# Optimization experiments

Hardware: AMD Instinct MI355X
Metric: run time of the kernel (lower is better)

The kernel has to match this reference:

```python
import jax, jax.numpy as jnp
import numpy as np

B, DIM, H, W = 4, 512, 64, 64
HEADS = 8
MAX_FREQ = 10000.0


def _rope_cos_sin(h, w, head_dim, dtype):
    # 2D RoPE: first quarter of half_dim uses row position, second quarter uses col position
    half = head_dim // 2
    quarter = half // 2
    pos_h = jnp.arange(h, dtype=dtype)
    pos_w = jnp.arange(w, dtype=dtype)
    gh, gw = jnp.meshgrid(pos_h, pos_w, indexing='ij')
    pos = jnp.stack([gh.ravel(), gw.ravel()], axis=-1)  # [N, 2]
    freqs = 1.0 / (MAX_FREQ ** (jnp.arange(quarter, dtype=dtype) / quarter))  # [quarter]
    ang_x = pos[:, 0:1] * freqs  # [N, quarter]
    ang_y = pos[:, 1:2] * freqs  # [N, quarter]
    cos = jnp.concatenate([jnp.cos(ang_x), jnp.cos(ang_y)], axis=-1)  # [N, half]
    sin = jnp.concatenate([jnp.sin(ang_x), jnp.sin(ang_y)], axis=-1)  # [N, half]
    return cos, sin


def _apply_rope(x, cos, sin):
    # x: [B, heads, N, head_dim]; cos/sin: [N, head_dim//2]
    d = x.shape[-1] // 2
    x1, x2 = x[..., :d], x[..., d:]
    return jnp.concatenate([x1 * cos - x2 * sin, x1 * sin + x2 * cos], axis=-1)


def setup_inputs() -> dict:
    key = jax.random.key(0)
    kx, kq, kp = jax.random.split(key, 3)
    x = jax.random.normal(kx, (B, DIM, H, W), dtype=jnp.float32)
    w_qkv = jax.random.normal(kq, (3 * DIM, DIM), dtype=jnp.float32) * (DIM ** -0.5)
    w_proj = jax.random.normal(kp, (DIM, DIM), dtype=jnp.float32) * (DIM ** -0.5)
    return {"x": x, "w_qkv": w_qkv, "w_proj": w_proj}


def reference(x, w_qkv, w_proj):
    Bb, C, Hh, Ww = x.shape
    heads = HEADS
    hd = C // heads
    N = Hh * Ww
    # 1x1 conv (bias-free) == channel-wise linear
    qkv = jnp.einsum('bchw,oc->bohw', x, w_qkv)  # [B, 3C, H, W]
    qkv = qkv.reshape(Bb, 3, heads, hd, Hh, Ww).transpose(1, 0, 2, 4, 5, 3)  # [3, B, heads, H, W, hd]
    q = qkv[0].reshape(Bb, heads, N, hd)
    k = qkv[1].reshape(Bb, heads, N, hd)
    v = qkv[2].reshape(Bb, heads, N, hd)
    cos, sin = _rope_cos_sin(Hh, Ww, hd, x.dtype)
    q = _apply_rope(q, cos, sin)
    k = _apply_rope(k, cos, sin)
    scale = hd ** -0.5
    attn = jax.nn.softmax(jnp.einsum('bhnd,bhmd->bhnm', q, k) * scale, axis=-1)  # [B, heads, N, N]
    out = jnp.einsum('bhnm,bhmd->bhnd', attn, v)  # [B, heads, N, hd]
    out = out.reshape(Bb, heads, Hh, Ww, hd).transpose(0, 1, 4, 2, 3).reshape(Bb, C, Hh, Ww)
    return jnp.einsum('bchw,oc->bohw', out, w_proj)
```

## Files before the change

kernel.cpp:

```cpp
#include <hip/hip_runtime.h>
#include <math.h>

#define B_    4
#define CDIM  512
#define HEADS 8
#define HD    64
#define NN    4096
#define QSZ   ((size_t)B_*HEADS*NN*HD)
#define SCALE_Q 0.18033688011112042f

typedef __attribute__((ext_vector_type(8))) short short8;
typedef __attribute__((ext_vector_type(4))) float f32x4;
typedef __attribute__((ext_vector_type(16))) float f32x16;
union U4S8 { uint4 u; short8 s; };

__device__ inline unsigned pk(float a, float b) {
    unsigned ua = __float_as_uint(a), ub = __float_as_uint(b);
    ua += 0x7FFFu + ((ua >> 16) & 1u);
    ub += 0x7FFFu + ((ub >> 16) & 1u);
    return (ua >> 16) | (ub & 0xFFFF0000u);
}
__device__ inline unsigned short bf16_1(float a) {
    unsigned ua = __float_as_uint(a);
    ua += 0x7FFFu + ((ua >> 16) & 1u);
    return (unsigned short)(ua >> 16);
}
__device__ inline unsigned cvtpk(float a, float b) {
    unsigned r;
    asm("v_cvt_pk_bf16_f32 %0, %1, %2" : "=v"(r) : "v"(a), "v"(b));
    return r;
}

__device__ inline void load_lds16(const unsigned short* g, unsigned short* l) {
    __builtin_amdgcn_global_load_lds(
        (const __attribute__((address_space(1))) unsigned int*)g,
        (__attribute__((address_space(3))) unsigned int*)l, 16, 0, 0);
}

__global__ void conv_w_kernel(const float* __restrict__ wq, const float* __restrict__ wp,
                              unsigned short* __restrict__ wqb, unsigned short* __restrict__ wpb) {
    int id = blockIdx.x * 256 + threadIdx.x;
    const float* src; unsigned short* dst; size_t off; float sc = 1.0f;
    if (id < 98304) { src = wq; dst = wqb; off = (size_t)id * 8; if (off < 262144) sc = SCALE_Q; }
    else            { src = wp; dst = wpb; off = (size_t)(id - 98304) * 8; }
    float4 a = *(const float4*)(src + off);
    float4 b = *(const float4*)(src + off + 4);
    uint4 u;
    u.x = pk(a.x * sc, a.y * sc); u.y = pk(a.z * sc, a.w * sc);
    u.z = pk(b.x * sc, b.y * sc); u.w = pk(b.z * sc, b.w * sc);
    *(uint4*)(dst + off) = u;
}

__global__ void rope_table_kernel(float* __restrict__ ct, float* __restrict__ st) {
    int id = blockIdx.x * 256 + threadIdx.x;
    int j = id >> 12, n = id & 4095;
    int i = j & 15;
    float pos = (j < 16) ? (float)(n >> 6) : (float)(n & 63);
    float freq = exp2f(-(float)i * 0.8304820237218406f);
    float ang = pos * freq;
    ct[id] = cosf(ang);
    st[id] = sinf(ang);
}

__global__ __launch_bounds__(256) void transpose_x_kernel(
        const float* __restrict__ x, unsigned short* __restrict__ xt) {
    __shared__ unsigned short T[64 * 72];
    int t = threadIdx.x;
    int b = blockIdx.z, c0 = blockIdx.y * 64, n0 = blockIdx.x * 64;
    const float* xb = x + ((size_t)b * CDIM + c0) * NN + n0;
    int crow = t >> 2, nseg = t & 3;
#pragma unroll
    for (int g = 0; g < 4; ++g) {
        float4 f = *(const float4*)(xb + (size_t)crow * NN + nseg * 16 + g * 4);
        int nb = nseg * 16 + g * 4;
        T[(nb + 0) * 72 + crow] = bf16_1(f.x);
        T[(nb + 1) * 72 + crow] = bf16_1(f.y);
        T[(nb + 2) * 72 + crow] = bf16_1(f.z);
        T[(nb + 3) * 72 + crow] = bf16_1(f.w);
    }
    __syncthreads();
    unsigned short* xo = xt + ((size_t)b * NN + n0) * CDIM + c0;
    int nrow = t >> 2, cseg = t & 3;
    uint4 u0 = *(uint4*)(T + nrow * 72 + cseg * 16);
    uint4 u1 = *(uint4*)(T + nrow * 72 + cseg * 16 + 8);
    *(uint4*)(xo + (size_t)nrow * CDIM + cseg * 16)     = u0;
    *(uint4*)(xo + (size_t)nrow * CDIM + cseg * 16 + 8) = u1;
}

__global__ __launch_bounds__(256, 2) void qkv_mfma_kernel(
        const unsigned short* __restrict__ xt, const unsigned short* __restrict__ wq,
        unsigned short* __restrict__ qbf, unsigned short* __restrict__ kbf,
        unsigned short* __restrict__ vt,
        const float* __restrict__ ct, const float* __restrict__ st) {
    __shared__ unsigned short smem[8192];
    int t = threadIdx.x;
    int lane = t & 63, w = t >> 6;
    int qlo = lane & 15, quad = lane >> 4;
    int b = blockIdx.z, o0 = blockIdx.y * 128, n0 = blockIdx.x * 128;
    const unsigned short* xb = xt + (size_t)b * NN * CDIM;
    int row = t >> 2, seg = t & 3;
    int wn = (w & 1) * 64, wo = (w >> 1) * 64;

    f32x4 acc[4][4];
#pragma unroll
    for (int i = 0; i < 4; ++i)
#pragma unroll
        for (int j = 0; j < 4; ++j) acc[i][j] = f32x4{0.f, 0.f, 0.f, 0.f};

    for (int k0 = 0; k0 < 512; k0 += 32) {
        __syncthreads();
        load_lds16(xb + (size_t)(n0 + row) * 512 + k0 + seg * 8,        smem + t * 8);
        load_lds16(xb + (size_t)(n0 + 64 + row) * 512 + k0 + seg * 8,   smem + 2048 + t * 8);
        load_lds16(wq + (size_t)(o0 + row) * 512 + k0 + seg * 8,        smem + 4096 + t * 8);
        load_lds16(wq + (size_t)(o0 + 64 + row) * 512 + k0 + seg * 8,   smem + 6144 + t * 8);
        __syncthreads();
        U4S8 af[4], bf[4];
#pragma unroll
        for (int mt = 0; mt < 4; ++mt)
            af[mt].u = *(const uint4*)(smem + (wn + 16 * mt + qlo) * 32 + quad * 8);
#pragma unroll
        for (int nt = 0; nt < 4; ++nt)
            bf[nt].u = *(const uint4*)(smem + 4096 + (wo + 16 * nt + qlo) * 32 + quad * 8);
#pragma unroll
        for (int mt = 0; mt < 4; ++mt)
#pragma unroll
            for (int nt = 0; nt < 4; ++nt)
                acc[mt][nt] = __builtin_amdgcn_mfma_f32_16x16x32_bf16(
                    af[mt].s, bf[nt].s, acc[mt][nt], 0, 0, 0);
    }

    int og = o0 + wo;
    int s = og >> 9;
    int h = (og & 511) >> 6;
    int bh = b * HEADS + h;
    if (s < 2) {
        unsigned short* dst = (s ? kbf : qbf) + (size_t)bh * NN * HD;
#pragma unroll
        for (int mt = 0; mt < 4; ++mt) {
            int nbase = n0 + wn + 16 * mt + 4 * quad;
#pragma unroll
            for (int ntp = 0; ntp < 2; ++ntp) {
                int j = 16 * ntp + qlo;
                float4 c4 = *(const float4*)(ct + (size_t)j * NN + nbase);
                float4 s4 = *(const float4*)(st + (size_t)j * NN + nbase);
                float cc[4] = {c4.x, c4.y, c4.z, c4.w};
                float ss[4] = {s4.x, s4.y, s4.z, s4.w};
#pragma unroll
                for (int r = 0; r < 4; ++r) {
                    float x1 = acc[mt][ntp][r], x2 = acc[mt][ntp + 2][r];
                    size_t base = (size_t)(nbase + r) * HD;
                    dst[base + j]      = bf16_1(x1 * cc[r] - x2 * ss[r]);
                    dst[base + j + 32] = bf16_1(x1 * ss[r] + x2 * cc[r]);
                }
            }
        }
    } else {
        unsigned short* dst = vt + (size_t)bh * HD * NN;
#pragma unroll
        for (int mt = 0; mt < 4; ++mt)
#pragma unroll
            for (int nt = 0; nt < 4; ++nt) {
                int d = 16 * nt + qlo;
                int n = n0 + wn + 16 * mt + 4 * quad;
                uint2 u;
                u.x = pk(acc[mt][nt][0], acc[mt][nt][1]);
                u.y = pk(acc[mt][nt][2], acc[mt][nt][3]);
                *(uint2*)(dst + (size_t)d * NN + n) = u;
            }
    }
}

__global__ __launch_bounds__(256, 2) void attn_kernel(
        const unsigned short* __restrict__ qbf, const unsigned short* __restrict__ kbf,
        const unsigned short* __restrict__ vt, unsigned short* __restrict__ aot) {
    __shared__ unsigned char smem[18432];
    int t = threadIdx.x;
    int lane = t & 63, w = t >> 6;
    int l31 = lane & 31, h = lane >> 5;
    int bb = blockIdx.z, hh = blockIdx.y;
    int bh = bb * HEADS + hh;
    int n0w = blockIdx.x * 256 + w * 64;

    U4S8 qf[2][4];
    const unsigned short* qg = qbf + ((size_t)bh * NN + n0w) * HD;
#pragma unroll
    for (int mtq = 0; mtq < 2; ++mtq)
#pragma unroll
        for (int ks = 0; ks < 4; ++ks)
            qf[mtq][ks].u = *(const uint4*)(qg + (size_t)(32 * mtq + l31) * 64 + 16 * ks + 8 * h);

    f32x16 Zv;
#pragma unroll
    for (int i = 0; i < 16; ++i) Zv[i] = 0.f;

    f32x16 O[2][2];
#pragma unroll
    for (int mtq = 0; mtq < 2; ++mtq)
#pragma unroll
        for (int ntd = 0; ntd < 2; ++ntd) O[mtq][ntd] = Zv;
    float Lsum[2] = {0.f, 0.f};

    const uint4* kg = (const uint4*)kbf + (size_t)bh * NN * 8;
    const uint4* vg = (const uint4*)vt  + (size_t)bh * 64 * 512;

    int rr0 = t >> 3, s8 = t & 7;
    int voff = 32 * (s8 >> 1) + 8 * (s8 & 1);
    uint4 kr0, kr1, vr0, vr1;
    kr0 = kg[(size_t)rr0 * 8 + s8];
    kr1 = kg[(size_t)(32 + rr0) * 8 + s8];
    vr0 = vg[(size_t)rr0 * 512 + s8];
    vr1 = vg[(size_t)(32 + rr0) * 512 + s8];

    for (int c = 0; c < NN / 64; ++c) {
        __syncthreads();
        *(uint4*)(smem + rr0 * 144 + s8 * 16)        = kr0;
        *(uint4*)(smem + (32 + rr0) * 144 + s8 * 16) = kr1;
        *(uint2*)(smem + 9216 + rr0 * 144 + voff)             = make_uint2(vr0.x, vr0.y);
        *(uint2*)(smem + 9216 + rr0 * 144 + voff + 16)        = make_uint2(vr0.z, vr0.w);
        *(uint2*)(smem + 9216 + (32 + rr0) * 144 + voff)      = make_uint2(vr1.x, vr1.y);
        *(uint2*)(smem + 9216 + (32 + rr0) * 144 + voff + 16) = make_uint2(vr1.z, vr1.w);
        __syncthreads();
        if (c + 1 < NN / 64) {
            int m0 = (c + 1) * 64;
            kr0 = kg[(size_t)(m0 + rr0) * 8 + s8];
            kr1 = kg[(size_t)(m0 + 32 + rr0) * 8 + s8];
            vr0 = vg[(size_t)rr0 * 512 + (m0 >> 3) + s8];
            vr1 = vg[(size_t)(32 + rr0) * 512 + (m0 >> 3) + s8];
        }

        f32x16 S[2][2];
        __builtin_amdgcn_s_setprio(1);
        {
            U4S8 ka0[2];
#pragma unroll
            for (int mtk = 0; mtk < 2; ++mtk)
                ka0[mtk].u = *(const uint4*)(smem + (32 * mtk + l31) * 144 + 16 * h);
#pragma unroll
            for (int mtk = 0; mtk < 2; ++mtk)
#pragma unroll
                for (int mtq = 0; mtq < 2; ++mtq)
                    S[mtk][mtq] = __builtin_amdgcn_mfma_f32_32x32x16_bf16(
                        ka0[mtk].s, qf[mtq][0].s, Zv, 0, 0, 0);
#pragma unroll
            for (int ks = 1; ks < 4; ++ks) {
                U4S8 ka[2];
#pragma unroll
                for (int mtk = 0; mtk < 2; ++mtk)
                    ka[mtk].u = *(const uint4*)(smem + (32 * mtk + l31) * 144 + 32 * ks + 16 * h);
#pragma unroll
                for (int mtk = 0; mtk < 2; ++mtk)
#pragma unroll
                    for (int mtq = 0; mtq < 2; ++mtq)
                        S[mtk][mtq] = __builtin_amdgcn_mfma_f32_32x32x16_bf16(
                            ka[mtk].s, qf[mtq][ks].s, S[mtk][mtq], 0, 0, 0);
            }
        }
        __builtin_amdgcn_s_setprio(0);

        U4S8 pa[2][2][2];
#pragma unroll
        for (int mtk = 0; mtk < 2; ++mtk)
#pragma unroll
            for (int mtq = 0; mtq < 2; ++mtq)
#pragma unroll
                for (int ksl = 0; ksl < 2; ++ksl) {
                    float p0 = __builtin_amdgcn_exp2f(S[mtk][mtq][8 * ksl + 0]);
                    float p1 = __builtin_amdgcn_exp2f(S[mtk][mtq][8 * ksl + 1]);
                    float p2 = __builtin_amdgcn_exp2f(S[mtk][mtq][8 * ksl + 2]);
                    float p3 = __builtin_amdgcn_exp2f(S[mtk][mtq][8 * ksl + 3]);
                    float p4 = __builtin_amdgcn_exp2f(S[mtk][mtq][8 * ksl + 4]);
                    float p5 = __builtin_amdgcn_exp2f(S[mtk][mtq][8 * ksl + 5]);
                    float p6 = __builtin_amdgcn_exp2f(S[mtk][mtq][8 * ksl + 6]);
                    float p7 = __builtin_amdgcn_exp2f(S[mtk][mtq][8 * ksl + 7]);
                    Lsum[mtq] += ((p0 + p1) + (p2 + p3)) + ((p4 + p5) + (p6 + p7));
                    pa[mtk][ksl][mtq].u.x = cvtpk(p0, p1);
                    pa[mtk][ksl][mtq].u.y = cvtpk(p2, p3);
                    pa[mtk][ksl][mtq].u.z = cvtpk(p4, p5);
                    pa[mtk][ksl][mtq].u.w = cvtpk(p6, p7);
                }

        __builtin_amdgcn_s_setprio(1);
#pragma unroll
        for (int mtk = 0; mtk < 2; ++mtk)
#pragma unroll
            for (int ksl = 0; ksl < 2; ++ksl)
#pragma unroll
                for (int ntd = 0; ntd < 2; ++ntd) {
                    U4S8 vb;
                    vb.u = *(const uint4*)(smem + 9216 + (32 * ntd + l31) * 144
                                           + 64 * mtk + 32 * ksl + 16 * h);
#pragma unroll
                    for (int mtq = 0; mtq < 2; ++mtq)
                        O[mtq][ntd] = __builtin_amdgcn_mfma_f32_32x32x16_bf16(
                            pa[mtk][ksl][mtq].s, vb.s, O[mtq][ntd], 0, 0, 0);
                }
        __builtin_amdgcn_s_setprio(0);
    }

    float Linv[2];
#pragma unroll
    for (int mtq = 0; mtq < 2; ++mtq) {
        float l = Lsum[mtq] + __shfl_xor(Lsum[mtq], 32, 64);
        Linv[mtq] = 1.0f / l;
    }
    __syncthreads();
    unsigned short* Tw = (unsigned short*)(smem + w * 4608);
    unsigned short* aob = aot + ((size_t)bb * NN) * CDIM + hh * 64;
#pragma unroll
    for (int mtq = 0; mtq < 2; ++mtq) {
        float iv[16];
#pragma unroll
        for (int r = 0; r < 16; ++r) {
            int src = (r & 3) + 8 * ((r >> 2) & 1) + 16 * (r >> 3) + 4 * h;
            iv[r] = __shfl(Linv[mtq], src, 64);
        }
#pragma unroll
        for (int rg = 0; rg < 2; ++rg) {
#pragma unroll
            for (int ntd = 0; ntd < 2; ++ntd)
#pragma unroll
                for (int rr = 0; rr < 8; ++rr) {
                    int r = 8 * rg + rr;
                    int q16 = (rr & 3) + 8 * (rr >> 2) + 4 * h;
                    Tw[q16 * 72 + 32 * ntd + l31] = bf16_1(O[mtq][ntd][r] * iv[r]);
                }
            int row = lane >> 2, cseg = lane & 3;
            uint4 u0 = *(uint4*)(Tw + row * 72 + cseg * 16);
            uint4 u1 = *(uint4*)(Tw + row * 72 + cseg * 16 + 8);
            unsigned short* arow = aob
                + (size_t)(n0w + 32 * mtq + 16 * rg + row) * CDIM + cseg * 16;
            *(uint4*)(arow)     = u0;
            *(uint4*)(arow + 8) = u1;
        }
    }
}

__global__ __launch_bounds__(256, 2) void proj_mfma_kernel(
        const unsigned short* __restrict__ aot, const unsigned short* __restrict__ wp,
        float* __restrict__ out) {
    __shared__ unsigned short smem[8192];
    int t = threadIdx.x;
    int lane = t & 63, w = t >> 6;
    int qlo = lane & 15, quad = lane >> 4;
    int b = blockIdx.z, o0 = blockIdx.y * 128, n0 = blockIdx.x * 128;
    const unsigned short* ab = aot + (size_t)b * NN * CDIM;
    int row = t >> 2, seg = t & 3;
    int wn = (w & 1) * 64, wo = (w >> 1) * 64;

    f32x4 acc[4][4];
#pragma unroll
    for (int i = 0; i < 4; ++i)
#pragma unroll
        for (int j = 0; j < 4; ++j) acc[i][j] = f32x4{0.f, 0.f, 0.f, 0.f};

    for (int k0 = 0; k0 < 512; k0 += 32) {
        __syncthreads();
        load_lds16(ab + (size_t)(n0 + row) * 512 + k0 + seg * 8,        smem + t * 8);
        load_lds16(ab + (size_t)(n0 + 64 + row) * 512 + k0 + seg * 8,   smem + 2048 + t * 8);
        load_lds16(wp + (size_t)(o0 + row) * 512 + k0 + seg * 8,        smem + 4096 + t * 8);
        load_lds16(wp + (size_t)(o0 + 64 + row) * 512 + k0 + seg * 8,   smem + 6144 + t * 8);
        __syncthreads();
        U4S8 af[4], bf[4];
#pragma unroll
        for (int mt = 0; mt < 4; ++mt)
            af[mt].u = *(const uint4*)(smem + (wn + 16 * mt + qlo) * 32 + quad * 8);
#pragma unroll
        for (int nt = 0; nt < 4; ++nt)
            bf[nt].u = *(const uint4*)(smem + 4096 + (wo + 16 * nt + qlo) * 32 + quad * 8);
#pragma unroll
        for (int mt = 0; mt < 4; ++mt)
#pragma unroll
            for (int nt = 0; nt < 4; ++nt)
                acc[mt][nt] = __builtin_amdgcn_mfma_f32_16x16x32_bf16(
                    af[mt].s, bf[nt].s, acc[mt][nt], 0, 0, 0);
    }

    float* ob = out + (size_t)b * CDIM * NN;
#pragma unroll
    for (int mt = 0; mt < 4; ++mt)
#pragma unroll
        for (int nt = 0; nt < 4; ++nt) {
            int o = o0 + wo + 16 * nt + qlo;
            int n = n0 + wn + 16 * mt + 4 * quad;
            *(float4*)(ob + (size_t)o * NN + n) = *(float4*)&acc[mt][nt];
        }
}

extern "C" void kernel_launch(void* const* d_in, const int* in_sizes, int n_in,
                              void* d_out, int out_size, void* d_ws, size_t ws_size,
                              hipStream_t stream) {
    const float* x      = (const float*)d_in[0];
    const float* w_qkv  = (const float*)d_in[1];
    const float* w_proj = (const float*)d_in[2];
    float* out = (float*)d_out;
    unsigned short* ws = (unsigned short*)d_ws;

    unsigned short* xt  = ws;
    unsigned short* qbf = xt  + QSZ;
    unsigned short* kbf = qbf + QSZ;
    unsigned short* vt  = kbf + QSZ;
    unsigned short* aot = vt  + QSZ;
    unsigned short* wqb = aot + QSZ;
    unsigned short* wpb = wqb + 786432;
    float* ct = (float*)(wpb + 262144);
    float* st = ct + 32 * 4096;

    conv_w_kernel<<<512, 256, 0, stream>>>(w_qkv, w_proj, wqb, wpb);
    rope_table_kernel<<<512, 256, 0, stream>>>(ct, st);
    transpose_x_kernel<<<dim3(64, 8, B_), 256, 0, stream>>>(x, xt);
    qkv_mfma_kernel<<<dim3(32, 12, B_), 256, 0, stream>>>(xt, wqb, qbf, kbf, vt, ct, st);
    attn_kernel<<<dim3(NN / 256, HEADS, B_), 256, 0, stream>>>(qbf, kbf, vt, aot);
    proj_mfma_kernel<<<dim3(32, 4, B_), 256, 0, stream>>>(aot, wpb, out);
}
```

Baseline: 291.9 us.

## Double-buffer K/V tiles in LDS with a single barrier per iteration

The attention kernel now keeps two LDS buffers for the K/V tiles. It writes the next tile into the alternate buffer after the current tile's MFMA work, so each iteration needs one __syncthreads instead of two. Global loads use incrementing pointers and run two tiles ahead. This doubles LDS use to 36 KB per block, which could limit occupancy alongside the two-blocks launch bound. The LDS writes now follow the compute rather than overlapping it.

```diff
diff --git a/kernel.cpp b/kernel.cpp
--- a/kernel.cpp
+++ b/kernel.cpp
@@ -173,7 +173,7 @@
 __global__ __launch_bounds__(256, 2) void attn_kernel(
         const unsigned short* __restrict__ qbf, const unsigned short* __restrict__ kbf,
         const unsigned short* __restrict__ vt, unsigned short* __restrict__ aot) {
-    __shared__ unsigned char smem[18432];
+    __shared__ unsigned char smem[36864];
     int t = threadIdx.x;
     int lane = t & 63, w = t >> 6;
     int l31 = lane & 31, h = lane >> 5;
@@ -205,28 +205,33 @@
 
     int rr0 = t >> 3, s8 = t & 7;
     int voff = 32 * (s8 >> 1) + 8 * (s8 & 1);
-    uint4 kr0, kr1, vr0, vr1;
-    kr0 = kg[(size_t)rr0 * 8 + s8];
-    kr1 = kg[(size_t)(32 + rr0) * 8 + s8];
-    vr0 = vg[(size_t)rr0 * 512 + s8];
-    vr1 = vg[(size_t)(32 + rr0) * 512 + s8];
+
+    const uint4* kp0 = kg + rr0 * 8 + s8;
+    const uint4* kp1 = kg + (32 + rr0) * 8 + s8;
+    const uint4* vp0 = vg + rr0 * 512 + s8;
+    const uint4* vp1 = vg + (32 + rr0) * 512 + s8;
+
+    unsigned char* kd0 = smem + rr0 * 144 + s8 * 16;
+    unsigned char* kd1 = smem + (32 + rr0) * 144 + s8 * 16;
+    unsigned char* vd0 = smem + 9216 + rr0 * 144 + voff;
+    unsigned char* vd1 = smem + 9216 + (32 + rr0) * 144 + voff;
+
+    uint4 kr0 = kp0[0], kr1 = kp1[0], vr0 = vp0[0], vr1 = vp1[0];
+    kp0 += 512; kp1 += 512; vp0 += 8; vp1 += 8;
+    *(uint4*)(kd0) = kr0;
+    *(uint4*)(kd1) = kr1;
+    *(uint2*)(vd0)      = make_uint2(vr0.x, vr0.y);
+    *(uint2*)(vd0 + 16) = make_uint2(vr0.z, vr0.w);
+    *(uint2*)(vd1)      = make_uint2(vr1.x, vr1.y);
+    *(uint2*)(vd1 + 16) = make_uint2(vr1.z, vr1.w);
+    kr0 = kp0[0]; kr1 = kp1[0]; vr0 = vp0[0]; vr1 = vp1[0];
+    kp0 += 512; kp1 += 512; vp0 += 8; vp1 += 8;
+    __syncthreads();
 
     for (int c = 0; c < NN / 64; ++c) {
-        __syncthreads();
-        *(uint4*)(smem + rr0 * 144 + s8 * 16)        = kr0;
-        *(uint4*)(smem + (32 + rr0) * 144 + s8 * 16) = kr1;
-        *(uint2*)(smem + 9216 + rr0 * 144 + voff)             = make_uint2(vr0.x, vr0.y);
-        *(uint2*)(smem + 9216 + rr0 * 144 + voff + 16)        = make_uint2(vr0.z, vr0.w);
-        *(uint2*)(smem + 9216 + (32 + rr0) * 144 + voff)      = make_uint2(vr1.x, vr1.y);
-        *(uint2*)(smem + 9216 + (32 + rr0) * 144 + voff + 16) = make_uint2(vr1.z, vr1.w);
-        __syncthreads();
-        if (c + 1 < NN / 64) {
-            int m0 = (c + 1) * 64;
-            kr0 = kg[(size_t)(m0 + rr0) * 8 + s8];
-            kr1 = kg[(size_t)(m0 + 32 + rr0) * 8 + s8];
-            vr0 = vg[(size_t)rr0 * 512 + (m0 >> 3) + s8];
-            vr1 = vg[(size_t)(32 + rr0) * 512 + (m0 >> 3) + s8];
-        }
+        int bo = (c & 1) * 18432;
+        const unsigned char* kb  = smem + bo;
+        const unsigned char* vbb = smem + bo + 9216;
 
         f32x16 S[2][2];
         __builtin_amdgcn_s_setprio(1);
@@ -234,7 +239,7 @@
             U4S8 ka0[2];
 #pragma unroll
             for (int mtk = 0; mtk < 2; ++mtk)
-                ka0[mtk].u = *(const uint4*)(smem + (32 * mtk + l31) * 144 + 16 * h);
+                ka0[mtk].u = *(const uint4*)(kb + (32 * mtk + l31) * 144 + 16 * h);
 #pragma unroll
             for (int mtk = 0; mtk < 2; ++mtk)
 #pragma unroll
@@ -246,7 +251,7 @@
                 U4S8 ka[2];
 #pragma unroll
                 for (int mtk = 0; mtk < 2; ++mtk)
-                    ka[mtk].u = *(const uint4*)(smem + (32 * mtk + l31) * 144 + 32 * ks + 16 * h);
+                    ka[mtk].u = *(const uint4*)(kb + (32 * mtk + l31) * 144 + 32 * ks + 16 * h);
 #pragma unroll
                 for (int mtk = 0; mtk < 2; ++mtk)
 #pragma unroll
@@ -287,7 +292,7 @@
 #pragma unroll
                 for (int ntd = 0; ntd < 2; ++ntd) {
                     U4S8 vb;
-                    vb.u = *(const uint4*)(smem + 9216 + (32 * ntd + l31) * 144
+                    vb.u = *(const uint4*)(vbb + (32 * ntd + l31) * 144
                                            + 64 * mtk + 32 * ksl + 16 * h);
 #pragma unroll
                     for (int mtq = 0; mtq < 2; ++mtq)
@@ -295,6 +300,21 @@
                             pa[mtk][ksl][mtq].s, vb.s, O[mtq][ntd], 0, 0, 0);
                 }
         __builtin_amdgcn_s_setprio(0);
+
+        if (c < NN / 64 - 1) {
+            int bo2 = ((c + 1) & 1) * 18432;
+            *(uint4*)(kd0 + bo2) = kr0;
+            *(uint4*)(kd1 + bo2) = kr1;
+            *(uint2*)(vd0 + bo2)      = make_uint2(vr0.x, vr0.y);
+            *(uint2*)(vd0 + bo2 + 16) = make_uint2(vr0.z, vr0.w);
+            *(uint2*)(vd1 + bo2)      = make_uint2(vr1.x, vr1.y);
+            *(uint2*)(vd1 + bo2 + 16) = make_uint2(vr1.z, vr1.w);
+            if (c < NN / 64 - 2) {
+                kr0 = kp0[0]; kr1 = kp1[0]; vr0 = vp0[0]; vr1 = vp1[0];
+                kp0 += 512; kp1 += 512; vp0 += 8; vp1 += 8;
+            }
+        }
+        __syncthreads();
     }
 
     float Linv[2];
@@ -303,7 +323,6 @@
         float l = Lsum[mtq] + __shfl_xor(Lsum[mtq], 32, 64);
         Linv[mtq] = 1.0f / l;
     }
-    __syncthreads();
     unsigned short* Tw = (unsigned short*)(smem + w * 4608);
     unsigned short* aob = aot + ((size_t)bb * NN) * CDIM + hh * 64;
 #pragma unroll
```

Result: no change. 288.0 us (-1.3%).
